# Optimization experiments

Measured on AMD Instinct MI355X. Metric: run time of the kernel, lower is better.

Reference implementation:

```python
import jax, jax.numpy as jnp
import numpy as np


def setup_inputs() -> dict:
    key = jax.random.key(0)
    kq, kk, kv = jax.random.split(key, 3)
    B, H, S, D = 2, 16, 2048, 64
    q = jax.random.normal(kq, (B, H, S, D), dtype=jnp.float32)
    k = jax.random.normal(kk, (B, H, S, D), dtype=jnp.float32)
    v = jax.random.normal(kv, (B, H, S, D), dtype=jnp.float32)
    return {"q": q, "k": k, "v": v}


def reference(q, k, v):
    # q,k,v: [B,H,S,D]
    d_tensor = q.shape[-1]
    scale = 1.0 / jnp.sqrt(jnp.asarray(d_tensor, dtype=q.dtype))
    # score: [B,H,S,S] -- full unfused score matrix, as in the original
    score = jnp.einsum("bhsd,bhtd->bhst", q, k) * scale
    score = jax.nn.softmax(score, axis=-1)
    out = jnp.einsum("bhst,bhtd->bhsd", score, v)
    return (out, score)
```

## Files before the change

kernel.cpp:

```cpp
#include <hip/hip_runtime.h>
#include <hip/hip_bf16.h>

#define S_LEN 2048
#define D_DIM 64
#define NBH   32
#define NE    ((size_t)NBH * S_LEN * D_DIM)

#define QB    64
#define CHK   64
#define NCHK  (S_LEN / CHK)

#define QSCALE 0.180336880146f

typedef __attribute__((ext_vector_type(4)))  float f32x4;
typedef __attribute__((ext_vector_type(16))) float f32x16;
typedef __attribute__((ext_vector_type(8)))  short s16x8;
typedef __attribute__((ext_vector_type(2)))  int   i32x2;

union FU { float f; unsigned int u; };
union PU { unsigned int u[4]; s16x8 v; };

__device__ __forceinline__ float bf2f(unsigned short h){
    FU x; x.u = ((unsigned int)h) << 16; return x.f;
}
__device__ __forceinline__ unsigned short f2bf(float f){
    __hip_bfloat16 h = __float2bfloat16(f);
    return __builtin_bit_cast(unsigned short, h);
}
__device__ __forceinline__ s16x8 cvt8(const float* p, float s){
    f32x4 a = *(const f32x4*)p, b = *(const f32x4*)(p + 4);
    s16x8 f;
    f[0]=(short)f2bf(a[0]*s); f[1]=(short)f2bf(a[1]*s); f[2]=(short)f2bf(a[2]*s); f[3]=(short)f2bf(a[3]*s);
    f[4]=(short)f2bf(b[0]*s); f[5]=(short)f2bf(b[1]*s); f[6]=(short)f2bf(b[2]*s); f[7]=(short)f2bf(b[3]*s);
    return f;
}
__device__ __forceinline__ float fexp2(float x){
    return __builtin_amdgcn_exp2f(fminf(x, 86.0f));
}

typedef __attribute__((address_space(3))) unsigned short lds_us;
typedef __attribute__((address_space(1))) const unsigned short glb_us;
__device__ __forceinline__ void gl16(const unsigned short* g, unsigned short* l){
    __builtin_amdgcn_global_load_lds((glb_us*)g, (lds_us*)l, 16, 0, 0);
}

__device__ __forceinline__ void barrier_lgkm(){
    asm volatile("s_waitcnt lgkmcnt(0)" ::: "memory");
    __builtin_amdgcn_s_barrier();
    __builtin_amdgcn_sched_barrier(0);
}

__device__ __forceinline__ void plswap(unsigned int& a, unsigned int& b){
#if __has_builtin(__builtin_amdgcn_permlane32_swap)
    i32x2 r = __builtin_amdgcn_permlane32_swap((int)a, (int)b, false, false);
    a = (unsigned int)r[0];
    b = (unsigned int)r[1];
#else
    const int ad = ((threadIdx.x & 63) ^ 32) * 4;
    const int ax = __builtin_amdgcn_ds_bpermute(ad, (int)a);
    const int bx = __builtin_amdgcn_ds_bpermute(ad, (int)b);
    const bool hi = (threadIdx.x & 32) != 0;
    unsigned int na = hi ? (unsigned int)bx : a;
    unsigned int nb = hi ? b : (unsigned int)ax;
    a = na; b = nb;
#endif
}

__global__ __launch_bounds__(256)
void cvt_bf16_kernel(const float* __restrict__ src, unsigned short* __restrict__ dst,
                     float scale, int n8)
{
    int i = blockIdx.x * 256 + threadIdx.x;
    if (i >= n8) return;
    *(s16x8*)(dst + (size_t)i * 8) = cvt8(src + (size_t)i * 8, scale);
}

__global__ __launch_bounds__(256)
void transpose_v_kernel(const float* __restrict__ V, unsigned short* __restrict__ Vt)
{
    __shared__ float tile[64][65];
    const int bh = blockIdx.y;
    const int s0 = blockIdx.x * 64;
    const int t  = threadIdx.x;
    const int r  = t >> 2;
    const int cs = (t & 3) * 16;

    const float* src = V + ((size_t)bh * S_LEN + s0 + r) * D_DIM + cs;
    #pragma unroll
    for (int j = 0; j < 16; j += 4){
        f32x4 v = *(const f32x4*)(src + j);
        tile[r][cs + j + 0] = v[0]; tile[r][cs + j + 1] = v[1];
        tile[r][cs + j + 2] = v[2]; tile[r][cs + j + 3] = v[3];
    }
    __syncthreads();
    s16x8 o0, o1;
    #pragma unroll
    for (int j = 0; j < 8; ++j)  o0[j] = (short)f2bf(tile[cs + j][r]);
    #pragma unroll
    for (int j = 0; j < 8; ++j)  o1[j] = (short)f2bf(tile[cs + 8 + j][r]);
    unsigned short* dst = Vt + ((size_t)bh * D_DIM + r) * S_LEN + s0 + cs;
    *(s16x8*)dst       = o0;
    *(s16x8*)(dst + 8) = o1;
}

__global__ __launch_bounds__(128, 2)
void sdpa_fused(const unsigned short* __restrict__ Qb,
                const unsigned short* __restrict__ Kb,
                const unsigned short* __restrict__ Vt,
                float* __restrict__ Out, float* __restrict__ Score)
{
    __shared__ unsigned short kbuf[2][CHK * D_DIM];
    __shared__ unsigned short vbuf[2][D_DIM * CHK];

    const int id  = blockIdx.x;
    const int j   = id >> 3;
    const int bh  = (id & 7) * 4 + (j >> 5);
    const int qt  = j & 31;

    const int tid = threadIdx.x;
    const int w   = tid >> 6;
    const int l   = tid & 63;
    const int h   = l >> 5;
    const int q32 = l & 31;
    const int qrow = qt * QB + w * 32;

    const unsigned short* Kbh = Kb + (size_t)bh * S_LEN * D_DIM;
    const unsigned short* Vbh = Vt + (size_t)bh * D_DIM * S_LEN;

    auto stageK = [&](int c, int b){
        #pragma unroll
        for (int i = 0; i < 4; ++i){
            const int slot = i*128 + w*64 + l;
            const int row  = slot >> 3;
            const int us   = (slot & 7) ^ (row & 7);
            gl16(Kbh + ((size_t)(c*CHK + row)) * D_DIM + us*8,
                 &kbuf[b][(i*128 + w*64) * 8]);
        }
    };

    auto loadK = [&](int c, s16x8* kr){
        #pragma unroll
        for (int i = 0; i < 4; ++i){
            const int slot = i*128 + w*64 + l;
            const int row  = slot >> 3;
            const int u    = slot & 7;
            kr[i] = *(const s16x8*)(Kbh + ((size_t)(c*CHK + row)) * D_DIM + u*8);
        }
    };
    auto loadV = [&](int c, s16x8* vr){
        #pragma unroll
        for (int i = 0; i < 4; ++i){
            const int slot = i*128 + w*64 + l;
            const int row  = slot >> 3;
            const int u    = slot & 7;
            vr[i] = *(const s16x8*)(Vbh + (size_t)row * S_LEN + c*CHK + u*8);
        }
    };
    auto writeKV = [&](int b, const s16x8* kr, const s16x8* vr){
        #pragma unroll
        for (int i = 0; i < 4; ++i){
            const int slot = i*128 + w*64 + l;
            const int row  = slot >> 3;
            const int u    = slot & 7;
            *(s16x8*)&kbuf[b][row*D_DIM + ((u ^ (row & 7)) * 8)] = kr[i];
            *(s16x8*)&vbuf[b][row*CHK  + ((u ^ (row & 7)) * 8)] = vr[i];
        }
    };

    s16x8 qB[4];
    {
        const unsigned short* qp = Qb + ((size_t)bh * S_LEN + qrow + q32) * D_DIM + h*8;
        #pragma unroll
        for (int s = 0; s < 4; ++s) qB[s] = *(const s16x8*)(qp + s*16);
    }

    float lsum = 0.f;
    stageK(0, 0);
    __syncthreads();
    for (int c = 0; c < NCHK; ++c){
        if (c + 1 < NCHK) stageK(c + 1, (c + 1) & 1);
        const unsigned short* kb = &kbuf[c & 1][0];
        #pragma unroll
        for (int kt = 0; kt < 2; ++kt){
            const int row = kt*32 + q32;
            f32x16 acc = {0.f,0.f,0.f,0.f,0.f,0.f,0.f,0.f,0.f,0.f,0.f,0.f,0.f,0.f,0.f,0.f};
            #pragma unroll
            for (int s = 0; s < 4; ++s){
                const int su = (2*s + h) ^ (row & 7);
                const s16x8 a = *(const s16x8*)(kb + row*D_DIM + su*8);
                acc = __builtin_amdgcn_mfma_f32_32x32x16_bf16(a, qB[s], acc, 0, 0, 0);
            }
            #pragma unroll
            for (int r = 0; r < 16; ++r)
                lsum += fexp2(acc[r]);
        }
        __syncthreads();
    }
    lsum += __shfl_xor(lsum, 32, 64);
    const float invl = 1.0f / lsum;

    float invreg[16];
    #pragma unroll
    for (int r = 0; r < 16; ++r){
        const int qa = (r & 3) + 8*(r >> 2);
        invreg[r] = __shfl(invl, qa + 4*h, 64);
    }

    f32x16 oacc[2];
    oacc[0] = (f32x16){0.f,0.f,0.f,0.f,0.f,0.f,0.f,0.f,0.f,0.f,0.f,0.f,0.f,0.f,0.f,0.f};
    oacc[1] = oacc[0];

    s16x8 krg[4], vrg[4];
    loadK(0, krg); loadV(0, vrg);
    writeKV(0, krg, vrg);
    barrier_lgkm();

    float* sbase = Score + ((size_t)bh * S_LEN + qrow + 4*h) * S_LEN + q32;

    for (int c = 0; c < NCHK; ++c){
        if (c + 1 < NCHK){
            loadK(c + 1, krg); loadV(c + 1, vrg);
            __builtin_amdgcn_sched_barrier(0);
        }
        const unsigned short* kb = &kbuf[c & 1][0];
        const unsigned short* vb = &vbuf[c & 1][0];

        #pragma unroll
        for (int kt = 0; kt < 2; ++kt){
            const int row = kt*32 + q32;
            f32x16 acc  = {0.f,0.f,0.f,0.f,0.f,0.f,0.f,0.f,0.f,0.f,0.f,0.f,0.f,0.f,0.f,0.f};
            f32x16 acc2 = acc;
            #pragma unroll
            for (int s = 0; s < 4; ++s){
                const int su = (2*s + h) ^ (row & 7);
                const s16x8 a = *(const s16x8*)(kb + row*D_DIM + su*8);
                acc  = __builtin_amdgcn_mfma_f32_32x32x16_bf16(a, qB[s], acc,  0, 0, 0);
                acc2 = __builtin_amdgcn_mfma_f32_32x32x16_bf16(qB[s], a, acc2, 0, 0, 0);
            }

            #pragma unroll
            for (int r = 0; r < 16; ++r){
                const int qa = (r & 3) + 8*(r >> 2);
                const float e = fexp2(acc2[r]) * invreg[r];
                __builtin_nontemporal_store(e, sbase + (size_t)qa * S_LEN + c*CHK + kt*32);
            }

            float e[16];
            #pragma unroll
            for (int r = 0; r < 16; ++r) e[r] = fexp2(acc[r]);

            unsigned int pk[8];
            #pragma unroll
            for (int p = 0; p < 8; ++p)
                pk[p] = (unsigned int)f2bf(e[2*p]) | ((unsigned int)f2bf(e[2*p+1]) << 16);

            plswap(pk[0], pk[2]);
            plswap(pk[1], pk[3]);
            plswap(pk[4], pk[6]);
            plswap(pk[5], pk[7]);
            PU p0, p1;
            p0.u[0] = pk[0]; p0.u[1] = pk[1]; p0.u[2] = pk[2]; p0.u[3] = pk[3];
            p1.u[0] = pk[4]; p1.u[1] = pk[5]; p1.u[2] = pk[6]; p1.u[3] = pk[7];

            #pragma unroll
            for (int dt = 0; dt < 2; ++dt){
                const int d   = dt*32 + q32;
                const int su0 = (kt*4 + h)     ^ (d & 7);
                const int su1 = (kt*4 + 2 + h) ^ (d & 7);
                const s16x8 v0 = *(const s16x8*)(vb + d*CHK + su0*8);
                const s16x8 v1 = *(const s16x8*)(vb + d*CHK + su1*8);
                oacc[dt] = __builtin_amdgcn_mfma_f32_32x32x16_bf16(v0, p0.v, oacc[dt], 0, 0, 0);
                oacc[dt] = __builtin_amdgcn_mfma_f32_32x32x16_bf16(v1, p1.v, oacc[dt], 0, 0, 0);
            }
        }

        if (c + 1 < NCHK){
            writeKV((c + 1) & 1, krg, vrg);
            barrier_lgkm();
        }
    }

    float* orow = Out + ((size_t)bh * S_LEN + qrow + q32) * D_DIM;
    #pragma unroll
    for (int dt = 0; dt < 2; ++dt){
        #pragma unroll
        for (int g = 0; g < 4; ++g){
            f32x4 o = { oacc[dt][4*g+0]*invl, oacc[dt][4*g+1]*invl,
                        oacc[dt][4*g+2]*invl, oacc[dt][4*g+3]*invl };
            *(f32x4*)(orow + dt*32 + 4*h + 8*g) = o;
        }
    }
}

__global__ __launch_bounds__(256)
void sdpa_naive(const float* __restrict__ Q, const float* __restrict__ K,
                const float* __restrict__ V, float* __restrict__ Out,
                float* __restrict__ Score)
{
    const int bh = blockIdx.y;
    const int qi = blockIdx.x;
    __shared__ float srow[S_LEN];
    __shared__ float qs[D_DIM];
    __shared__ float red[256];
    const int t = threadIdx.x;
    const float* qp = Q + ((size_t)bh * S_LEN + qi) * D_DIM;
    if (t < D_DIM) qs[t] = qp[t] * 0.125f;
    __syncthreads();
    float m = -1e30f;
    for (int k = t; k < S_LEN; k += 256){
        const float* kp = K + ((size_t)bh * S_LEN + k) * D_DIM;
        float s = 0.f;
        for (int d = 0; d < D_DIM; ++d) s += qs[d] * kp[d];
        srow[k] = s;
        m = fmaxf(m, s);
    }
    red[t] = m; __syncthreads();
    for (int o = 128; o; o >>= 1){ if (t < o) red[t] = fmaxf(red[t], red[t + o]); __syncthreads(); }
    m = red[0]; __syncthreads();
    float sum = 0.f;
    for (int k = t; k < S_LEN; k += 256){ float e = __expf(srow[k] - m); srow[k] = e; sum += e; }
    red[t] = sum; __syncthreads();
    for (int o = 128; o; o >>= 1){ if (t < o) red[t] += red[t + o]; __syncthreads(); }
    const float inv = 1.0f / red[0];
    float* sout = Score + ((size_t)bh * S_LEN + qi) * S_LEN;
    for (int k = t; k < S_LEN; k += 256) sout[k] = srow[k] * inv;
    if (t < D_DIM){
        float acc = 0.f;
        for (int k = 0; k < S_LEN; ++k) acc += srow[k] * V[((size_t)bh * S_LEN + k) * D_DIM + t];
        Out[((size_t)bh * S_LEN + qi) * D_DIM + t] = acc * inv;
    }
}

extern "C" void kernel_launch(void* const* d_in, const int* in_sizes, int n_in,
                              void* d_out, int out_size, void* d_ws, size_t ws_size,
                              hipStream_t stream)
{
    const float* q = (const float*)d_in[0];
    const float* k = (const float*)d_in[1];
    const float* v = (const float*)d_in[2];
    float* out   = (float*)d_out;
    float* score = out + NE;

    if (ws_size >= 3 * NE * sizeof(unsigned short)){
        unsigned short* Qb = (unsigned short*)d_ws;
        unsigned short* Kb = Qb + NE;
        unsigned short* Vt = Kb + NE;
        const int n8 = (int)(NE / 8);
        cvt_bf16_kernel<<<(n8 + 255) / 256, 256, 0, stream>>>(q, Qb, QSCALE, n8);
        cvt_bf16_kernel<<<(n8 + 255) / 256, 256, 0, stream>>>(k, Kb, 1.0f, n8);
        transpose_v_kernel<<<dim3(S_LEN / 64, NBH), 256, 0, stream>>>(v, Vt);
        sdpa_fused<<<(S_LEN / QB) * NBH, 128, 0, stream>>>(Qb, Kb, Vt, out, score);
    } else {
        sdpa_naive<<<dim3(S_LEN, NBH), 256, 0, stream>>>(q, k, v, out, score);
    }
}
```

Before: 172.6 us.

## Fuse PV accumulation into row-sum pass and make score pass K-only

Moves the P·V accumulation into the first pass, which now computes row sums and unnormalized output together, using async global-to-LDS staging for both K and V. The output is normalized and written before the second pass, which then only recomputes QK^T, writes normalized scores, and stages only K. The exp2 clamp is also removed. The aim is to shorten the critical second pass that carries the large score writes, at the cost of more LDS traffic and register pressure in the first pass. Dropping the clamp risks overflow for large logits, since no max is subtracted.

```diff
diff --git a/kernel.cpp b/kernel.cpp
--- a/kernel.cpp
+++ b/kernel.cpp
@@ -35,7 +35,7 @@
     return f;
 }
 __device__ __forceinline__ float fexp2(float x){
-    return __builtin_amdgcn_exp2f(fminf(x, 86.0f));
+    return __builtin_amdgcn_exp2f(x);
 }
 
 typedef __attribute__((address_space(3))) unsigned short lds_us;
@@ -137,6 +137,16 @@
                  &kbuf[b][(i*128 + w*64) * 8]);
         }
     };
+    auto stageV = [&](int c, int b){
+        #pragma unroll
+        for (int i = 0; i < 4; ++i){
+            const int slot = i*128 + w*64 + l;
+            const int row  = slot >> 3;
+            const int us   = (slot & 7) ^ (row & 7);
+            gl16(Vbh + (size_t)row * S_LEN + c*CHK + us*8,
+                 &vbuf[b][(i*128 + w*64) * 8]);
+        }
+    };
 
     auto loadK = [&](int c, s16x8* kr){
         #pragma unroll
@@ -147,23 +157,13 @@
             kr[i] = *(const s16x8*)(Kbh + ((size_t)(c*CHK + row)) * D_DIM + u*8);
         }
     };
-    auto loadV = [&](int c, s16x8* vr){
-        #pragma unroll
-        for (int i = 0; i < 4; ++i){
-            const int slot = i*128 + w*64 + l;
-            const int row  = slot >> 3;
-            const int u    = slot & 7;
-            vr[i] = *(const s16x8*)(Vbh + (size_t)row * S_LEN + c*CHK + u*8);
-        }
-    };
-    auto writeKV = [&](int b, const s16x8* kr, const s16x8* vr){
+    auto writeK = [&](int b, const s16x8* kr){
         #pragma unroll
         for (int i = 0; i < 4; ++i){
             const int slot = i*128 + w*64 + l;
             const int row  = slot >> 3;
             const int u    = slot & 7;
             *(s16x8*)&kbuf[b][row*D_DIM + ((u ^ (row & 7)) * 8)] = kr[i];
-            *(s16x8*)&vbuf[b][row*CHK  + ((u ^ (row & 7)) * 8)] = vr[i];
         }
     };
 
@@ -175,11 +175,17 @@
     }
 
     float lsum = 0.f;
+    f32x16 oacc[2];
+    oacc[0] = (f32x16){0.f,0.f,0.f,0.f,0.f,0.f,0.f,0.f,0.f,0.f,0.f,0.f,0.f,0.f,0.f,0.f};
+    oacc[1] = oacc[0];
+
     stageK(0, 0);
+    stageV(0, 0);
     __syncthreads();
     for (int c = 0; c < NCHK; ++c){
-        if (c + 1 < NCHK) stageK(c + 1, (c + 1) & 1);
+        if (c + 1 < NCHK){ stageK(c + 1, (c + 1) & 1); stageV(c + 1, (c + 1) & 1); }
         const unsigned short* kb = &kbuf[c & 1][0];
+        const unsigned short* vb = &vbuf[c & 1][0];
         #pragma unroll
         for (int kt = 0; kt < 2; ++kt){
             const int row = kt*32 + q32;
@@ -190,70 +196,14 @@
                 const s16x8 a = *(const s16x8*)(kb + row*D_DIM + su*8);
                 acc = __builtin_amdgcn_mfma_f32_32x32x16_bf16(a, qB[s], acc, 0, 0, 0);
             }
-            #pragma unroll
-            for (int r = 0; r < 16; ++r)
-                lsum += fexp2(acc[r]);
-        }
-        __syncthreads();
-    }
-    lsum += __shfl_xor(lsum, 32, 64);
-    const float invl = 1.0f / lsum;
-
-    float invreg[16];
-    #pragma unroll
-    for (int r = 0; r < 16; ++r){
-        const int qa = (r & 3) + 8*(r >> 2);
-        invreg[r] = __shfl(invl, qa + 4*h, 64);
-    }
-
-    f32x16 oacc[2];
-    oacc[0] = (f32x16){0.f,0.f,0.f,0.f,0.f,0.f,0.f,0.f,0.f,0.f,0.f,0.f,0.f,0.f,0.f,0.f};
-    oacc[1] = oacc[0];
-
-    s16x8 krg[4], vrg[4];
-    loadK(0, krg); loadV(0, vrg);
-    writeKV(0, krg, vrg);
-    barrier_lgkm();
-
-    float* sbase = Score + ((size_t)bh * S_LEN + qrow + 4*h) * S_LEN + q32;
-
-    for (int c = 0; c < NCHK; ++c){
-        if (c + 1 < NCHK){
-            loadK(c + 1, krg); loadV(c + 1, vrg);
-            __builtin_amdgcn_sched_barrier(0);
-        }
-        const unsigned short* kb = &kbuf[c & 1][0];
-        const unsigned short* vb = &vbuf[c & 1][0];
-
-        #pragma unroll
-        for (int kt = 0; kt < 2; ++kt){
-            const int row = kt*32 + q32;
-            f32x16 acc  = {0.f,0.f,0.f,0.f,0.f,0.f,0.f,0.f,0.f,0.f,0.f,0.f,0.f,0.f,0.f,0.f};
-            f32x16 acc2 = acc;
-            #pragma unroll
-            for (int s = 0; s < 4; ++s){
-                const int su = (2*s + h) ^ (row & 7);
-                const s16x8 a = *(const s16x8*)(kb + row*D_DIM + su*8);
-                acc  = __builtin_amdgcn_mfma_f32_32x32x16_bf16(a, qB[s], acc,  0, 0, 0);
-                acc2 = __builtin_amdgcn_mfma_f32_32x32x16_bf16(qB[s], a, acc2, 0, 0, 0);
-            }
-
-            #pragma unroll
-            for (int r = 0; r < 16; ++r){
-                const int qa = (r & 3) + 8*(r >> 2);
-                const float e = fexp2(acc2[r]) * invreg[r];
-                __builtin_nontemporal_store(e, sbase + (size_t)qa * S_LEN + c*CHK + kt*32);
-            }
-
             float e[16];
             #pragma unroll
-            for (int r = 0; r < 16; ++r) e[r] = fexp2(acc[r]);
+            for (int r = 0; r < 16; ++r){ e[r] = fexp2(acc[r]); lsum += e[r]; }
 
             unsigned int pk[8];
             #pragma unroll
             for (int p = 0; p < 8; ++p)
                 pk[p] = (unsigned int)f2bf(e[2*p]) | ((unsigned int)f2bf(e[2*p+1]) << 16);
-
             plswap(pk[0], pk[2]);
             plswap(pk[1], pk[3]);
             plswap(pk[4], pk[6]);
@@ -273,21 +223,63 @@
                 oacc[dt] = __builtin_amdgcn_mfma_f32_32x32x16_bf16(v1, p1.v, oacc[dt], 0, 0, 0);
             }
         }
+        __syncthreads();
+    }
+    lsum += __shfl_xor(lsum, 32, 64);
+    const float invl = 1.0f / lsum;
+
+    float invreg[16];
+    #pragma unroll
+    for (int r = 0; r < 16; ++r){
+        const int qa = (r & 3) + 8*(r >> 2);
+        invreg[r] = __shfl(invl, qa + 4*h, 64);
+    }
+
+    {
+        float* orow = Out + ((size_t)bh * S_LEN + qrow + q32) * D_DIM;
+        #pragma unroll
+        for (int dt = 0; dt < 2; ++dt){
+            #pragma unroll
+            for (int g = 0; g < 4; ++g){
+                f32x4 o = { oacc[dt][4*g+0]*invl, oacc[dt][4*g+1]*invl,
+                            oacc[dt][4*g+2]*invl, oacc[dt][4*g+3]*invl };
+                __builtin_nontemporal_store(o, (f32x4*)(orow + dt*32 + 4*h + 8*g));
+            }
+        }
+    }
+
+    s16x8 krg[4];
+    loadK(0, krg);
+    writeK(0, krg);
+    barrier_lgkm();
+
+    float* sbase = Score + ((size_t)bh * S_LEN + qrow + 4*h) * S_LEN + q32;
+
+    for (int c = 0; c < NCHK; ++c){
+        if (c + 1 < NCHK) loadK(c + 1, krg);
+        const unsigned short* kb = &kbuf[c & 1][0];
+
+        #pragma unroll
+        for (int kt = 0; kt < 2; ++kt){
+            const int row = kt*32 + q32;
+            f32x16 acc2 = {0.f,0.f,0.f,0.f,0.f,0.f,0.f,0.f,0.f,0.f,0.f,0.f,0.f,0.f,0.f,0.f};
+            #pragma unroll
+            for (int s = 0; s < 4; ++s){
+                const int su = (2*s + h) ^ (row & 7);
+                const s16x8 a = *(const s16x8*)(kb + row*D_DIM + su*8);
+                acc2 = __builtin_amdgcn_mfma_f32_32x32x16_bf16(qB[s], a, acc2, 0, 0, 0);
+            }
+            #pragma unroll
+            for (int r = 0; r < 16; ++r){
+                const int qa = (r & 3) + 8*(r >> 2);
+                const float e = fexp2(acc2[r]) * invreg[r];
+                __builtin_nontemporal_store(e, sbase + (size_t)qa * S_LEN + c*CHK + kt*32);
+            }
+        }
 
         if (c + 1 < NCHK){
-            writeKV((c + 1) & 1, krg, vrg);
+            writeK((c + 1) & 1, krg);
             barrier_lgkm();
-        }
-    }
-
-    float* orow = Out + ((size_t)bh * S_LEN + qrow + q32) * D_DIM;
-    #pragma unroll
-    for (int dt = 0; dt < 2; ++dt){
-        #pragma unroll
-        for (int g = 0; g < 4; ++g){
-            f32x4 o = { oacc[dt][4*g+0]*invl, oacc[dt][4*g+1]*invl,
-                        oacc[dt][4*g+2]*invl, oacc[dt][4*g+3]*invl };
-            *(f32x4*)(orow + dt*32 + 4*h + 8*g) = o;
         }
     }
 }
```

After: 185.1 us. 1.07x slower.
